# Kernel optimization log

Hardware: AMD Instinct MI355X
Metric: run time of the kernel (lower is better)

## Reference

```python
import jax, jax.numpy as jnp
import numpy as np

B, C, D, H, W = 2, 32, 16, 64, 64
SCALER = 8
CK = C // SCALER  # qk channels = 4


def setup_inputs() -> dict:
    key = jax.random.key(0)
    ks = jax.random.split(key, 8)
    s = 0.05
    return {
        "x": jax.random.normal(ks[0], (B, C, D, H, W), dtype=jnp.float32),
        "Wk": jax.random.normal(ks[1], (CK, C), dtype=jnp.float32) * s,
        "bk": jax.random.normal(ks[2], (CK,), dtype=jnp.float32) * s,
        "Wq": jax.random.normal(ks[3], (CK, C), dtype=jnp.float32) * s,
        "bq": jax.random.normal(ks[4], (CK,), dtype=jnp.float32) * s,
        "Wv": jax.random.normal(ks[5], (C, C), dtype=jnp.float32) * s,
        "bv": jax.random.normal(ks[6], (C,), dtype=jnp.float32) * s,
        "gamma": jnp.ones((1,), dtype=jnp.float32),
    }


def _proj(x, Wt, b):
    # 1x1x1 Conv3d == channel matmul: (o,c) x (b,c,d,h,w) -> (b,o,d,h,w)
    y = jnp.einsum('oc,bcdhw->bodhw', Wt, x) + b[None, :, None, None, None]
    return y


def reference(x, Wk, bk, Wq, bq, Wv, bv, gamma):
    b, c, d, h, w = x.shape
    hw = h * w
    xk = _proj(x, Wk, bk).reshape(b, -1, hw)   # (b, ck*d, hw)
    xq = _proj(x, Wq, bq).reshape(b, -1, hw)   # (b, ck*d, hw)
    xv = _proj(x, Wv, bv).reshape(b, -1, hw)   # (b, c*d,  hw)
    # dot[b,i,j] = sum_e xk[b,e,i] * xq[b,e,j]  -> (b, hw, hw)
    dot = jnp.einsum('bei,bej->bij', xk, xq)
    att = jax.nn.softmax(dot, axis=-1)          # softmax over last dim
    # x_a[b,m,i] = sum_j xv[b,m,j] * att[b,i,j]
    x_a = jnp.einsum('bmj,bij->bmi', xv, att)
    x_a = x_a.reshape(b, c, d, h, w)
    return gamma[0] * x + x_a
```

## Files before the change

kernel.cpp:

```cpp
#include <hip/hip_runtime.h>
#include <hip/hip_bf16.h>

#define B_   2
#define C_   32
#define D_   16
#define HW_  4096
#define CK_  4
#define E_   64
#define M_   512
#define NO_  40
#define JC_  4

typedef __attribute__((ext_vector_type(8)))  short bf16x8;
typedef __attribute__((ext_vector_type(16))) float f32x16;

union U4 { unsigned int u[4]; bf16x8 v; };

__device__ __forceinline__ short f2bf(float f) {
    __hip_bfloat16 h = __float2bfloat16(f);
    return *reinterpret_cast<short*>(&h);
}
__device__ __forceinline__ unsigned short f2bfu(float f) {
    __hip_bfloat16 h = __float2bfloat16(f);
    return *reinterpret_cast<unsigned short*>(&h);
}

__global__ void prep_kernel(
    const float* __restrict__ Wk, const float* __restrict__ bk,
    const float* __restrict__ Wq, const float* __restrict__ bq,
    const float* __restrict__ Wv, const float* __restrict__ bv,
    float* __restrict__ Wt, float* __restrict__ bt)
{
    int t = threadIdx.x;
    for (int i = t; i < NO_*C_; i += 256) {
        int o = i / C_, c = i % C_;
        float val = (o < 4) ? Wk[o*C_ + c]
                  : (o < 8) ? Wq[(o-4)*C_ + c]
                            : Wv[(o-8)*C_ + c];
        Wt[c*NO_ + o] = val;
    }
    if (t < NO_) bt[t] = (t < 4) ? bk[t] : (t < 8) ? bq[t-4] : bv[t-8];
}

__global__ __launch_bounds__(256) void proj_kernel(
    const float* __restrict__ x,
    const float* __restrict__ Wt, const float* __restrict__ bt,
    short* __restrict__ xk, short* __restrict__ xq,
    __hip_bfloat16* __restrict__ v)
{
    __shared__ short s_t[2][64*72];
    const int t   = threadIdx.x;
    const int pin = t & 63, dq = t >> 6;
    const int pb  = blockIdx.x & 63;
    const int db  = (blockIdx.x >> 6) & 3;
    const int b   = blockIdx.x >> 8;
    const int d   = db*4 + dq;
    const int p   = pb*64 + pin;

    float xc[C_];
    #pragma unroll
    for (int c = 0; c < C_; ++c)
        xc[c] = x[(((size_t)(b*C_ + c)*D_ + d)*HW_) + p];

    float acc[NO_];
    {
        const float4* bt4 = (const float4*)bt;
        #pragma unroll
        for (int k = 0; k < 10; ++k) {
            float4 bb = bt4[k];
            acc[4*k+0] = bb.x; acc[4*k+1] = bb.y; acc[4*k+2] = bb.z; acc[4*k+3] = bb.w;
        }
    }
    const float4* Wt4 = (const float4*)Wt;
    #pragma unroll
    for (int c = 0; c < C_; ++c) {
        float xv = xc[c];
        #pragma unroll
        for (int k = 0; k < 10; ++k) {
            float4 w = Wt4[c*10 + k];
            acc[4*k+0] += w.x * xv;
            acc[4*k+1] += w.y * xv;
            acc[4*k+2] += w.z * xv;
            acc[4*k+3] += w.w * xv;
        }
    }

    #pragma unroll
    for (int o = 0; o < CK_; ++o) {
        int e = o*D_ + d;
        s_t[0][pin*72 + e] = f2bf(acc[o]);
        s_t[1][pin*72 + e] = f2bf(acc[4+o]);
    }
    #pragma unroll
    for (int o = 0; o < C_; ++o)
        v[((size_t)b*M_ + (o*D_ + d))*HW_ + p] = __float2bfloat16(acc[8+o]);

    __syncthreads();
    const int row = t >> 2, quar = t & 3;
    size_t gbase = ((size_t)b*HW_ + pb*64 + row)*E_ + quar*16;
    const short* src = &s_t[0][row*72 + quar*16];
    *(uint4*)(xk + gbase)     = *(const uint4*)(src);
    *(uint4*)(xk + gbase + 8) = *(const uint4*)(src + 8);
    src = &s_t[1][row*72 + quar*16];
    *(uint4*)(xq + gbase)     = *(const uint4*)(src);
    *(uint4*)(xq + gbase + 8) = *(const uint4*)(src + 8);
}

__device__ __forceinline__ void load_lds16(const short* g, short* l) {
    __builtin_amdgcn_global_load_lds((const __attribute__((address_space(1))) void*)g,
                                     (__attribute__((address_space(3))) void*)l,
                                     16, 0, 0);
}

__global__ __launch_bounds__(256, 4) void attn_kernel(
    const short* __restrict__ xk_, const short* __restrict__ xq_,
    const short* __restrict__ v_,
    unsigned short* __restrict__ Op, float* __restrict__ lw)
{
    __shared__ short s_xq[2][2048];
    __shared__ short s_v [2][4096];

    const int t    = threadIdx.x;
    const int lane = t & 63;
    const int w    = t >> 6;
    const int h    = lane >> 5;
    const int c    = lane & 31;

    const int cls  = blockIdx.x & 7;
    const int b    = cls >> 2, mg = cls & 3;
    const int rest = blockIdx.x >> 3;
    const int ig   = rest & 31;
    const int jc   = rest >> 5;
    const int i0   = ig*128 + w*32;
    const int jbase = jc*(HW_/JC_);

    const short* xk_g = xk_ + (size_t)b*HW_*E_;
    const short* xq_g = xq_ + (size_t)b*HW_*E_;
    const short* v_g  = v_  + (size_t)b*M_*HW_ + (size_t)mg*128*HW_;

    bf16x8 kb[4];
    #pragma unroll
    for (int s = 0; s < 4; ++s)
        kb[s] = *(const bf16x8*)(xk_g + (size_t)(i0 + c)*E_ + s*16 + h*8);

    f32x16 acc[4];
    #pragma unroll
    for (int mt = 0; mt < 4; ++mt)
        #pragma unroll
        for (int r = 0; r < 16; ++r) acc[mt][r] = 0.f;
    float l_part = 0.f;

    auto stage = [&](int buf, int j0) {
        {
            int r_ = w*8 + (lane>>3), cc = (lane&7) ^ (r_&7);
            load_lds16(xq_g + (size_t)(j0 + r_)*E_ + cc*8, &s_xq[buf][w*512]);
        }
        #pragma unroll
        for (int k = 0; k < 2; ++k) {
            int r0 = w*32 + k*16;
            int r_ = r0 + (lane>>2);
            int g  = (lane&3) ^ ((r_>>1)&3);
            load_lds16(v_g + (size_t)r_*HW_ + j0 + g*8, &s_v[buf][r0*32]);
        }
    };

    stage(0, jbase);
    __syncthreads();

    for (int it = 0; it < (HW_/JC_)/32; ++it) {
        const int cur = it & 1;
        if (it + 1 < (HW_/JC_)/32)
            stage(cur^1, jbase + (it+1)*32);

        f32x16 st;
        #pragma unroll
        for (int r = 0; r < 16; ++r) st[r] = 0.f;
        #pragma unroll
        for (int s = 0; s < 4; ++s) {
            int slot = (s*2 + h) ^ (c & 7);
            bf16x8 a1 = *(const bf16x8*)(&s_xq[cur][c*64 + slot*8]);
            st = __builtin_amdgcn_mfma_f32_32x32x16_bf16(a1, kb[s], st, 0, 0, 0);
        }

        unsigned int dq[8], pd[8];
        #pragma unroll
        for (int qd = 0; qd < 8; ++qd) {
            float p0 = __expf(st[2*qd]);
            float p1 = __expf(st[2*qd+1]);
            l_part += p0 + p1;
            union { float f; unsigned int u; } ua, ub;
            ua.f = p0; ub.f = p1;
            dq[qd] = __builtin_amdgcn_perm(ub.u, ua.u, 0x07060302);
        }
        #pragma unroll
        for (int qd = 0; qd < 8; ++qd) pd[qd] = __shfl_xor(dq[qd], 32, 64);

        #pragma unroll
        for (int s2 = 0; s2 < 2; ++s2) {
            U4 a2;
            if (s2 == 0) {
                a2.u[0] = h ? pd[2] : dq[0];
                a2.u[1] = h ? pd[3] : dq[1];
                a2.u[2] = h ? dq[2] : pd[0];
                a2.u[3] = h ? dq[3] : pd[1];
            } else {
                a2.u[0] = h ? pd[6] : dq[4];
                a2.u[1] = h ? pd[7] : dq[5];
                a2.u[2] = h ? dq[6] : pd[4];
                a2.u[3] = h ? dq[7] : pd[5];
            }
            #pragma unroll
            for (int mt = 0; mt < 4; ++mt) {
                int rowm = mt*32 + c;
                int slot = (s2*2 + h) ^ ((rowm>>1)&3);
                bf16x8 vb = *(const bf16x8*)(&s_v[cur][rowm*32 + slot*8]);
                acc[mt] = __builtin_amdgcn_mfma_f32_32x32x16_bf16(a2.v, vb, acc[mt], 0, 0, 0);
            }
        }
        __syncthreads();
    }

    float l = l_part + __shfl_xor(l_part, 32, 64);
    if (h == 0 && mg == 0)
        lw[(size_t)(jc*B_ + b)*HW_ + i0 + c] = l;

    const size_t opb = ((size_t)(jc*B_ + b)*M_ + mg*128)*HW_;
    #pragma unroll
    for (int mt = 0; mt < 4; ++mt) {
        size_t rb = opb + (size_t)(mt*32 + c)*HW_ + i0;
        #pragma unroll
        for (int g = 0; g < 4; ++g) {
            ushort4 s4;
            s4.x = f2bfu(acc[mt][4*g+0]);
            s4.y = f2bfu(acc[mt][4*g+1]);
            s4.z = f2bfu(acc[mt][4*g+2]);
            s4.w = f2bfu(acc[mt][4*g+3]);
            *(ushort4*)(Op + rb + 8*g + 4*h) = s4;
        }
    }
}

__global__ __launch_bounds__(256) void reduce_kernel(
    const float* __restrict__ x, const float* __restrict__ gamma_p,
    const unsigned short* __restrict__ Op, const float* __restrict__ lw,
    float* __restrict__ out)
{
    size_t idx = ((size_t)blockIdx.x*256 + threadIdx.x)*4;
    int i = idx & (HW_-1);
    size_t bm = idx >> 12;
    int m = bm & (M_-1);
    int b = (int)(bm >> 9);

    float4 o = {0.f,0.f,0.f,0.f};
    float4 l = {0.f,0.f,0.f,0.f};
    #pragma unroll
    for (int jc = 0; jc < JC_; ++jc) {
        ushort4 ov = *(const ushort4*)(Op + ((size_t)(jc*B_ + b)*M_ + m)*HW_ + i);
        o.x += __uint_as_float((unsigned int)ov.x << 16);
        o.y += __uint_as_float((unsigned int)ov.y << 16);
        o.z += __uint_as_float((unsigned int)ov.z << 16);
        o.w += __uint_as_float((unsigned int)ov.w << 16);
        float4 lv = *(const float4*)(lw + (size_t)(jc*B_ + b)*HW_ + i);
        l.x += lv.x; l.y += lv.y; l.z += lv.z; l.w += lv.w;
    }
    const float gamma = gamma_p[0];
    float4 xv = *(const float4*)(x + idx);
    float4 r;
    r.x = gamma*xv.x + o.x / l.x;
    r.y = gamma*xv.y + o.y / l.y;
    r.z = gamma*xv.z + o.z / l.z;
    r.w = gamma*xv.w + o.w / l.w;
    *(float4*)(out + idx) = r;
}

extern "C" void kernel_launch(void* const* d_in, const int* in_sizes, int n_in,
                              void* d_out, int out_size, void* d_ws, size_t ws_size,
                              hipStream_t stream)
{
    const float* x     = (const float*)d_in[0];
    const float* Wk    = (const float*)d_in[1];
    const float* bk    = (const float*)d_in[2];
    const float* Wq    = (const float*)d_in[3];
    const float* bq    = (const float*)d_in[4];
    const float* Wv    = (const float*)d_in[5];
    const float* bv    = (const float*)d_in[6];
    const float* gamma = (const float*)d_in[7];
    float* out = (float*)d_out;

    char* ws = (char*)d_ws;
    short*          xk = (short*)(ws);
    short*          xq = (short*)(ws + (1<<20));
    short*          v  = (short*)(ws + (2<<20));
    float*          Wt = (float*)(ws + (10<<20));
    float*          bt = (float*)(ws + (10<<20) + 5120);
    unsigned short* Op = (unsigned short*)(ws + (10<<20) + 8192);
    float*          lw = (float*)(ws + (10<<20) + 8192
                                  + (size_t)JC_*B_*M_*HW_*2);

    prep_kernel<<<1, 256, 0, stream>>>(Wk, bk, Wq, bq, Wv, bv, Wt, bt);
    proj_kernel<<<B_*(D_/4)*(HW_/64), 256, 0, stream>>>(x, Wt, bt, xk, xq,
                                                        (__hip_bfloat16*)v);
    attn_kernel<<<8*32*JC_, 256, 0, stream>>>(xk, xq, v, Op, lw);
    reduce_kernel<<<(B_*M_*HW_)/(256*4), 256, 0, stream>>>(x, gamma, Op, lw, out);
}
```

Before: 179.0 us.

## Compute 1x1x1 projections with bf16 MFMA instead of scalar FMA

Rewrites the projection kernel so that each wave computes the 40 output channels for 32 pixels with 32x32x16 bf16 MFMA instructions, using bf16 weights packed by the prep kernel and padded to 64 rows. Input x is converted to bf16 by truncation when it is packed into MFMA operands. The grid doubles to 32-pixel tiles and the k/q transpose through LDS shrinks. This removes the scalar FMA work and the float weight loads, at the cost of bf16 rounding of x and the weights before the projection.

After: 167.0 us. 6.7% less time.

```diff
diff --git a/kernel.cpp b/kernel.cpp
--- a/kernel.cpp
+++ b/kernel.cpp
@@ -8,7 +8,6 @@
 #define CK_  4
 #define E_   64
 #define M_   512
-#define NO_  40
 #define JC_  4
 
 typedef __attribute__((ext_vector_type(8)))  short bf16x8;
@@ -29,81 +28,85 @@
     const float* __restrict__ Wk, const float* __restrict__ bk,
     const float* __restrict__ Wq, const float* __restrict__ bq,
     const float* __restrict__ Wv, const float* __restrict__ bv,
-    float* __restrict__ Wt, float* __restrict__ bt)
+    short* __restrict__ Wall, float* __restrict__ ball)
 {
     int t = threadIdx.x;
-    for (int i = t; i < NO_*C_; i += 256) {
-        int o = i / C_, c = i % C_;
-        float val = (o < 4) ? Wk[o*C_ + c]
-                  : (o < 8) ? Wq[(o-4)*C_ + c]
-                            : Wv[(o-8)*C_ + c];
-        Wt[c*NO_ + o] = val;
-    }
-    if (t < NO_) bt[t] = (t < 4) ? bk[t] : (t < 8) ? bq[t-4] : bv[t-8];
+    for (int i = t; i < 64*C_; i += 256) {
+        int o = i >> 5, cc = i & 31;
+        float val = (o < 32) ? Wv[o*C_ + cc]
+                  : (o < 36) ? Wk[(o-32)*C_ + cc]
+                  : (o < 40) ? Wq[(o-36)*C_ + cc] : 0.f;
+        Wall[o*C_ + cc] = f2bf(val);
+    }
+    if (t < 64)
+        ball[t] = (t < 32) ? bv[t] : (t < 36) ? bk[t-32] : (t < 40) ? bq[t-36] : 0.f;
 }
 
 __global__ __launch_bounds__(256) void proj_kernel(
     const float* __restrict__ x,
-    const float* __restrict__ Wt, const float* __restrict__ bt,
+    const short* __restrict__ Wall, const float* __restrict__ ball,
     short* __restrict__ xk, short* __restrict__ xq,
     __hip_bfloat16* __restrict__ v)
 {
-    __shared__ short s_t[2][64*72];
-    const int t   = threadIdx.x;
-    const int pin = t & 63, dq = t >> 6;
-    const int pb  = blockIdx.x & 63;
-    const int db  = (blockIdx.x >> 6) & 3;
-    const int b   = blockIdx.x >> 8;
-    const int d   = db*4 + dq;
-    const int p   = pb*64 + pin;
-
-    float xc[C_];
-    #pragma unroll
-    for (int c = 0; c < C_; ++c)
-        xc[c] = x[(((size_t)(b*C_ + c)*D_ + d)*HW_) + p];
-
-    float acc[NO_];
-    {
-        const float4* bt4 = (const float4*)bt;
-        #pragma unroll
-        for (int k = 0; k < 10; ++k) {
-            float4 bb = bt4[k];
-            acc[4*k+0] = bb.x; acc[4*k+1] = bb.y; acc[4*k+2] = bb.z; acc[4*k+3] = bb.w;
-        }
-    }
-    const float4* Wt4 = (const float4*)Wt;
-    #pragma unroll
-    for (int c = 0; c < C_; ++c) {
-        float xv = xc[c];
-        #pragma unroll
-        for (int k = 0; k < 10; ++k) {
-            float4 w = Wt4[c*10 + k];
-            acc[4*k+0] += w.x * xv;
-            acc[4*k+1] += w.y * xv;
-            acc[4*k+2] += w.z * xv;
-            acc[4*k+3] += w.w * xv;
-        }
-    }
-
-    #pragma unroll
-    for (int o = 0; o < CK_; ++o) {
-        int e = o*D_ + d;
-        s_t[0][pin*72 + e] = f2bf(acc[o]);
-        s_t[1][pin*72 + e] = f2bf(acc[4+o]);
-    }
-    #pragma unroll
-    for (int o = 0; o < C_; ++o)
-        v[((size_t)b*M_ + (o*D_ + d))*HW_ + p] = __float2bfloat16(acc[8+o]);
-
+    __shared__ short s_k[32*16], s_q[32*16];
+    const int t    = threadIdx.x;
+    const int lane = t & 63;
+    const int w    = t >> 6;
+    const int h    = lane >> 5;
+    const int c    = lane & 31;
+
+    const int pt = blockIdx.x & 127;
+    const int dg = (blockIdx.x >> 7) & 3;
+    const int b  = blockIdx.x >> 9;
+    const int d  = dg*4 + w;
+    const int p0 = pt*32;
+
+    bf16x8 af[2][2];
+    #pragma unroll
+    for (int mt = 0; mt < 2; ++mt)
+        #pragma unroll
+        for (int s = 0; s < 2; ++s)
+            af[mt][s] = *(const bf16x8*)(Wall + (mt*32 + c)*C_ + s*16 + h*8);
+
+    U4 xb[2];
+    #pragma unroll
+    for (int s = 0; s < 2; ++s) {
+        #pragma unroll
+        for (int j = 0; j < 4; ++j) {
+            int c0 = s*16 + h*8 + 2*j;
+            union { float f; unsigned int u; } ua, ub;
+            ua.f = x[(((size_t)(b*C_ + c0  )*D_ + d)*HW_) + p0 + c];
+            ub.f = x[(((size_t)(b*C_ + c0+1)*D_ + d)*HW_) + p0 + c];
+            xb[s].u[j] = __builtin_amdgcn_perm(ub.u, ua.u, 0x07060302);
+        }
+    }
+
+    f32x16 a0, a1;
+    #pragma unroll
+    for (int r = 0; r < 16; ++r) { a0[r] = 0.f; a1[r] = 0.f; }
+    #pragma unroll
+    for (int s = 0; s < 2; ++s) {
+        a0 = __builtin_amdgcn_mfma_f32_32x32x16_bf16(af[0][s], xb[s].v, a0, 0, 0, 0);
+        a1 = __builtin_amdgcn_mfma_f32_32x32x16_bf16(af[1][s], xb[s].v, a1, 0, 0, 0);
+    }
+
+    #pragma unroll
+    for (int r = 0; r < 16; ++r) {
+        int o = (r & 3) + 8*(r >> 2) + 4*h;
+        v[((size_t)b*M_ + (o*D_ + d))*HW_ + p0 + c] = __float2bfloat16(a0[r] + ball[o]);
+    }
+
+    #pragma unroll
+    for (int r = 0; r < 4; ++r) {
+        if (h == 0) s_k[c*16 + w*4 + r] = f2bf(a1[r] + ball[32 + r]);
+        else        s_q[c*16 + w*4 + r] = f2bf(a1[r] + ball[36 + r]);
+    }
     __syncthreads();
-    const int row = t >> 2, quar = t & 3;
-    size_t gbase = ((size_t)b*HW_ + pb*64 + row)*E_ + quar*16;
-    const short* src = &s_t[0][row*72 + quar*16];
-    *(uint4*)(xk + gbase)     = *(const uint4*)(src);
-    *(uint4*)(xk + gbase + 8) = *(const uint4*)(src + 8);
-    src = &s_t[1][row*72 + quar*16];
-    *(uint4*)(xq + gbase)     = *(const uint4*)(src);
-    *(uint4*)(xq + gbase + 8) = *(const uint4*)(src + 8);
+
+    const int p = t >> 3, seg = t & 7;
+    size_t gb = ((size_t)b*HW_ + p0 + p)*E_ + dg*16 + seg*2;
+    *(unsigned int*)(xk + gb) = *(const unsigned int*)(&s_k[p*16 + seg*2]);
+    *(unsigned int*)(xq + gb) = *(const unsigned int*)(&s_q[p*16 + seg*2]);
 }
 
 __device__ __forceinline__ void load_lds16(const short* g, short* l) {
@@ -288,17 +291,17 @@
     float* out = (float*)d_out;
 
     char* ws = (char*)d_ws;
-    short*          xk = (short*)(ws);
-    short*          xq = (short*)(ws + (1<<20));
-    short*          v  = (short*)(ws + (2<<20));
-    float*          Wt = (float*)(ws + (10<<20));
-    float*          bt = (float*)(ws + (10<<20) + 5120);
-    unsigned short* Op = (unsigned short*)(ws + (10<<20) + 8192);
-    float*          lw = (float*)(ws + (10<<20) + 8192
-                                  + (size_t)JC_*B_*M_*HW_*2);
-
-    prep_kernel<<<1, 256, 0, stream>>>(Wk, bk, Wq, bq, Wv, bv, Wt, bt);
-    proj_kernel<<<B_*(D_/4)*(HW_/64), 256, 0, stream>>>(x, Wt, bt, xk, xq,
+    short*          xk   = (short*)(ws);
+    short*          xq   = (short*)(ws + (1<<20));
+    short*          v    = (short*)(ws + (2<<20));
+    short*          Wall = (short*)(ws + (10<<20));
+    float*          ball = (float*)(ws + (10<<20) + 4096);
+    unsigned short* Op   = (unsigned short*)(ws + (10<<20) + 8192);
+    float*          lw   = (float*)(ws + (10<<20) + 8192
+                                    + (size_t)JC_*B_*M_*HW_*2);
+
+    prep_kernel<<<1, 256, 0, stream>>>(Wk, bk, Wq, bq, Wv, bv, Wall, ball);
+    proj_kernel<<<B_*(D_/4)*(HW_/32), 256, 0, stream>>>(x, Wall, ball, xk, xq,
                                                         (__hip_bfloat16*)v);
     attn_kernel<<<8*32*JC_, 256, 0, stream>>>(xk, xq, v, Op, lw);
     reduce_kernel<<<(B_*M_*HW_)/(256*4), 256, 0, stream>>>(x, gamma, Op, lw, out);
```
